# Kernel tuning notes

Hardware: AMD Instinct MI355X
Metric: run time of the kernel (lower is better)

The kernel has to match this reference:

```python
import jax, jax.numpy as jnp
from jax import lax
import numpy as np

B, C, L, HOP = 16, 64, 16384, 256
KS = 3        # LVC / conv kernel size
DIL = 3       # static Conv1d dilation (init arg)
KL = L // HOP # kernel_length (number of conditioning frames)


def setup_inputs() -> dict:
    key = jax.random.key(0)
    k0, k1, k2, k3 = jax.random.split(key, 4)
    return {
        "hidden_states": jax.random.normal(k0, (B, C, L), jnp.float32),
        "kernel": jax.random.normal(k1, (B, C, 2 * C, KS, KL), jnp.float32) * 0.05,
        "bias": jax.random.normal(k2, (B, 2 * C, KL), jnp.float32) * 0.05,
        "conv_w": jax.random.normal(k3, (C, C, KS), jnp.float32) * 0.05,
        "conv_b": jnp.zeros((C,), jnp.float32),
        "hop_size": HOP,
    }


def _lvc(x, kernel, bias, hop_size):
    # location-variable convolution; forward() uses dilation=1 here
    b, c, length = x.shape
    _, _, out_ch, ksize, klen = kernel.shape
    pad = (ksize - 1) // 2
    xp = jnp.pad(x, ((0, 0), (0, 0), (pad, pad)))
    # sliding windows of size ksize, stride 1 -> (b, c, length, ksize)
    win = jnp.stack([xp[:, :, i:i + length] for i in range(ksize)], axis=-1)
    # split time into (kernel_length, hop_size) frames
    win = win.reshape(b, c, klen, hop_size, ksize)
    # per-frame conv kernel contraction
    o = jnp.einsum('bilsk,biokl->bols', win, kernel)  # (b, out_ch, klen, hop)
    o = o + bias[:, :, :, None]
    return o.reshape(b, out_ch, klen * hop_size)


def reference(hidden_states, kernel, bias, conv_w, conv_b, hop_size):
    slope = 0.2
    pad = DIL * (KS - 1) // 2
    residual = hidden_states
    h = jax.nn.leaky_relu(hidden_states, slope)
    h = lax.conv_general_dilated(
        h, conv_w, window_strides=(1,), padding=[(pad, pad)],
        rhs_dilation=(DIL,), dimension_numbers=('NCH', 'OIH', 'NCH'))
    h = h + conv_b[None, :, None]
    h = jax.nn.leaky_relu(h, slope)
    h = _lvc(h, kernel, bias, hop_size)
    c = residual.shape[1]
    h = jax.nn.sigmoid(h[:, :c, :]) * jnp.tanh(h[:, c:, :])  # GLU gate
    return residual + h
```

## Files before the change

### kernel.cpp

```cpp
#include <hip/hip_runtime.h>
#include <hip/hip_bf16.h>

#define TB 256

typedef __attribute__((ext_vector_type(8))) short short8;
typedef __attribute__((ext_vector_type(4))) unsigned int uint4v;
typedef __attribute__((ext_vector_type(4))) float f32x4;

#define KTF_BYTES 50331648ull
#define WS_NEED   (KTF_BYTES + 24576ull)

static __device__ __forceinline__ float lrelu(float v){ return v > 0.f ? v : 0.2f*v; }

static __device__ __forceinline__ unsigned int pack2(float lo, float hi){
    __hip_bfloat162 h = __float22bfloat162_rn(float2{lo, hi});
    unsigned int r;
    __builtin_memcpy(&r, &h, 4);
    return r;
}

static __device__ __forceinline__ float bf2f(unsigned int u16v){
    return __uint_as_float(u16v << 16);
}

static __device__ __forceinline__ float glu_gate(float a, float t){
    t = fminf(fmaxf(t, -10.f), 10.f);
    float u = __expf(-a);
    float v = __expf(2.0f * t);
    float den = (1.0f + u) * (v + 1.0f);
    return (v - 1.0f) * __builtin_amdgcn_rcpf(den);
}


__global__ __launch_bounds__(256, 4)
void ktf_transpose(const float* __restrict__ kern, unsigned int* __restrict__ ktf)
{
    __shared__ unsigned int tl32[128 * 65];
    const int tid = threadIdx.x;
    const int blk = blockIdx.x;
    const int k   = blk % 3;
    const int ci2 = (blk / 3) % 32;
    const int b   = blk / 96;
    const int kk  = k*2 + (ci2 >> 4);
    const int hi  = (ci2 >> 2) & 3;
    const int jp  = ci2 & 3;

    const float* src0 = kern + (size_t)b*1572864 + (size_t)ci2*49152 + k*64;
    #pragma unroll
    for (int it = 0; it < 8; ++it) {
        int p = tid + it*TB;
        int oc = p >> 4, fq = p & 15;
        const float* s = src0 + oc*192 + fq*4;
        float4 v0 = *(const float4*)(s);
        float4 v1 = *(const float4*)(s + 24576);
        unsigned int* d = tl32 + oc*65 + fq*4;
        d[0] = pack2(v0.x, v1.x);
        d[1] = pack2(v0.y, v1.y);
        d[2] = pack2(v0.z, v1.z);
        d[3] = pack2(v0.w, v1.w);
    }
    __syncthreads();

    const int l = tid & 63, wvv = tid >> 6;
    const int c = (kk*4 + jp)*4 + hi;
    const int oc0 = 2*l;
    const int slot0 = (oc0 < 64) ? ((oc0 >> 3)*16 + (oc0 & 7))
                                 : (((oc0 - 64) >> 3)*16 + 8 + ((oc0 - 64) & 7));
    unsigned int* dst = ktf + (size_t)(b*96 + c)*8192 + slot0;
    const int f0 = wvv*16;
    #pragma unroll
    for (int fi = 0; fi < 16; ++fi) {
        int f = f0 + fi;
        uint2 v;
        v.x = tl32[(oc0    )*65 + f];
        v.y = tl32[(oc0 + 1)*65 + f];
        *(uint2*)(dst + f*128) = v;
    }
}

__global__ __launch_bounds__(256, 4)
void wf_prep(const float* __restrict__ conv_w, unsigned int* __restrict__ wf)
{
    int u = blockIdx.x*TB + threadIdx.x;
    int ln = u & 63, mt = (u >> 6) & 3, jp = (u >> 8) & 3, kk = u >> 10;
    int lo = ln & 15, hi = ln >> 4;
    int m  = mt*16 + lo;
    int k  = kk >> 1, ci = (kk & 1)*32 + hi*8 + jp*2;
    float a0 = conv_w[m*192 + ci*3 + k];
    float a1 = conv_w[m*192 + (ci + 1)*3 + k];
    wf[u] = pack2(a0, a1);
}

#define LDS_HT   18432
#define LDS_BIAS 36864

__global__ __launch_bounds__(512, 6)
void fused_kernel(const float* __restrict__ x,
                  const float* __restrict__ bias,
                  const float* __restrict__ conv_b,
                  const unsigned int* __restrict__ ktf,
                  const unsigned int* __restrict__ wf,
                  float* __restrict__ out)
{
    __shared__ char lds[37376];
    float* bias_lds = (float*)(lds + LDS_BIAS);

    const int tid = threadIdx.x;
    const int blk = blockIdx.x;
    const int h = blk & 1;
    const int bf = blk >> 1;
    const int b = bf >> 6, f = bf & 63;
    const int t0 = f << 8;
    const int tb = t0 + h*128;
    const int ln = tid & 63, wv = tid >> 6;
    const int lo = ln & 15, hi = ln >> 4;
    const int mt = wv & 3, nth = wv >> 2;

    if (tid < 128) bias_lds[tid] = bias[(size_t)b*8192 + tid*64 + f];

    {
        const float* xb = x + ((size_t)b*64 + wv*8) * 16384;
        const int ts = tb - 12;
        const bool interior = (ts >= 0) & (ts + 143 < 16384);
        #pragma unroll
        for (int it = 0; it < 3; ++it) {
            int p = (it < 2) ? (ln + it*64) : (128 + ln);
            if (it < 2 || ln < 16) {
                int t = ts + p;
                float v[8];
                if (interior) {
                    #pragma unroll
                    for (int j = 0; j < 8; ++j) v[j] = xb[j*16384 + t];
                } else {
                    bool ok = (unsigned)t < 16384u;
                    #pragma unroll
                    for (int j = 0; j < 8; ++j) v[j] = ok ? xb[j*16384 + t] : 0.f;
                }
                unsigned int w0 = pack2(lrelu(v[0]), lrelu(v[1]));
                unsigned int w1 = pack2(lrelu(v[2]), lrelu(v[3]));
                unsigned int w2 = pack2(lrelu(v[4]), lrelu(v[5]));
                unsigned int w3 = pack2(lrelu(v[6]), lrelu(v[7]));
                int a = (p*128 + wv*16) ^ ((p & 7) << 4);
                *(uint4*)(lds + a) = make_uint4(w0, w1, w2, w3);
            }
        }
    }
    __syncthreads();

    {
        uint4v aw[6];
        #pragma unroll
        for (int kk = 0; kk < 6; ++kk) {
            int w0 = kk*1024 + mt*64 + ln;
            aw[kk].x = wf[w0      ]; aw[kk].y = wf[w0 + 256];
            aw[kk].z = wf[w0 + 512]; aw[kk].w = wf[w0 + 768];
        }
        float4 cb4 = *(const float4*)(conv_b + mt*16 + hi*4);
        const int n0  = nth ? 5 : 0;
        const int cnt = nth ? 4 : 5;
        int bqa[6];
        #pragma unroll
        for (int kk = 0; kk < 6; ++kk) {
            int row = n0*16 + lo + 3*(kk >> 1) + 1;
            int cib = (kk & 1)*32 + hi*8;
            bqa[kk] = (row*128 + cib*2) ^ ((row & 7) << 4);
        }
        int hta = LDS_HT + (((n0*16 + lo)*128 + (mt*16 + hi*4)*2) ^ ((lo & 7) << 4));
        int pos = tb + n0*16 + lo - 8;
        #pragma unroll 1
        for (int i = 0; i < cnt; ++i) {
            f32x4 acc = {0.f, 0.f, 0.f, 0.f};
            __builtin_amdgcn_s_setprio(1);
            #pragma unroll
            for (int kk = 0; kk < 6; ++kk) {
                short8 bq = *(const short8*)(lds + bqa[kk]);
                acc = __builtin_amdgcn_mfma_f32_16x16x32_bf16(
                        __builtin_bit_cast(short8, aw[kk]), bq, acc, 0, 0, 0);
            }
            __builtin_amdgcn_s_setprio(0);

            bool valid = (unsigned)pos < 16384u;
            unsigned int h01 = valid ? pack2(lrelu(acc[0] + cb4.x), lrelu(acc[1] + cb4.y)) : 0u;
            unsigned int h23 = valid ? pack2(lrelu(acc[2] + cb4.z), lrelu(acc[3] + cb4.w)) : 0u;
            unsigned int* d = (unsigned int*)(lds + hta);
            d[0] = h01; d[1] = h23;

            #pragma unroll
            for (int kk = 0; kk < 6; ++kk) bqa[kk] += 2048;
            hta += 2048; pos += 16;
        }
    }
    __syncthreads();

    {
        uint4v am[6];
        const unsigned int* kp = ktf + (size_t)b*786432 + hi*8192 + f*128 + wv*16 + lo;
        #pragma unroll
        for (int kk = 0; kk < 6; ++kk) {
            int o = kk*131072;
            am[kk].x = kp[o        ]; am[kk].y = kp[o + 32768];
            am[kk].z = kp[o + 65536]; am[kk].w = kp[o + 98304];
        }
        const int c0 = wv*8;
        const bool alane = hi < 2;
        const int chA = alane ? (c0 + hi*4) : (c0 + (hi - 2)*4 + 2);
        float bs0 = bias_lds[chA],      bs1 = bias_lds[chA + 1];
        float bt0 = bias_lds[chA + 64], bt1 = bias_lds[chA + 65];

        int bqa[6];
        #pragma unroll
        for (int kk = 0; kk < 6; ++kk) {
            int row = lo + 7 + (kk >> 1);
            int cib = (kk & 1)*32 + hi*8;
            bqa[kk] = LDS_HT + ((row*128 + cib*2) ^ ((row & 7) << 4));
        }
        int q  = lo + 12;
        int ra = (q*128 + chA*2) ^ ((q & 7) << 4);
        float* ob = out + ((size_t)b*64 + chA)*16384 + tb + lo;

        #pragma unroll 1
        for (int i = 0; i < 8; ++i) {
            f32x4 acc = {0.f, 0.f, 0.f, 0.f};
            __builtin_amdgcn_s_setprio(1);
            #pragma unroll
            for (int kk = 0; kk < 6; ++kk) {
                short8 bq = *(const short8*)(lds + bqa[kk]);
                acc = __builtin_amdgcn_mfma_f32_16x16x32_bf16(
                        __builtin_bit_cast(short8, am[kk]), bq, acc, 0, 0, 0);
            }
            __builtin_amdgcn_s_setprio(0);

            float q1 = alane ? acc[2] : acc[0];
            float q2 = alane ? acc[3] : acc[1];
            float r1 = __shfl_xor(q1, 32, 64);
            float r2 = __shfl_xor(q2, 32, 64);
            float sig0 = alane ? acc[0] : r1;
            float tan0 = alane ? r1 : acc[2];
            float sig1 = alane ? acc[1] : r2;
            float tan1 = alane ? r2 : acc[3];

            unsigned int rv = *(const unsigned int*)(lds + ra);
            float h0 = bf2f(rv & 0xFFFFu), h1 = bf2f(rv >> 16);
            float xr0 = h0 > 0.f ? h0 : 5.0f*h0;
            float xr1 = h1 > 0.f ? h1 : 5.0f*h1;

            float g0 = glu_gate(sig0 + bs0, tan0 + bt0);
            float g1 = glu_gate(sig1 + bs1, tan1 + bt1);
            ob[(size_t)i*16]           = xr0 + g0;
            ob[16384 + (size_t)i*16]   = xr1 + g1;

            #pragma unroll
            for (int kk = 0; kk < 6; ++kk) bqa[kk] += 2048;
            ra += 2048;
        }
    }
}

extern "C" void kernel_launch(void* const* d_in, const int* in_sizes, int n_in,
                              void* d_out, int out_size, void* d_ws, size_t ws_size,
                              hipStream_t stream)
{
    const float* x      = (const float*)d_in[0];
    const float* kern   = (const float*)d_in[1];
    const float* bias   = (const float*)d_in[2];
    const float* conv_b = (const float*)d_in[4];
    float* out = (float*)d_out;

    if (ws_size < WS_NEED) return;

    unsigned int* ktf = (unsigned int*)d_ws;
    unsigned int* wf  = (unsigned int*)((char*)d_ws + KTF_BYTES);

    wf_prep      <<<dim3(24),   dim3(TB), 0, stream>>>((const float*)d_in[3], wf);
    ktf_transpose<<<dim3(1536), dim3(TB), 0, stream>>>(kern, ktf);
    fused_kernel <<<dim3(2048), dim3(512), 0, stream>>>(x, bias, conv_b, ktf, wf, out);
    (void)in_sizes; (void)n_in; (void)out_size;
}
```

Before: 85.36 us.

## Switch conv and LVC matmuls to 32x32x16 MFMA with new operand layouts

Both the dilated conv stage and the per-frame LVC contraction now use 32x32x16 bf16 MFMA tiles instead of 16x16x32. The weight-prep and kernel-transpose kernels are rewritten so each lane fetches its A operand as one 16-byte vector load. The sigmoid and tanh rows now land in the same lane, which removes the cross-lane shuffle in the GLU epilogue. The intent is fewer MFMA issues, fewer scattered global loads and a cheaper epilogue. In exchange the accumulators grow to 16 registers, launch bounds occupancy drops from 6 to 4, the LDS swizzle changes, and the conv stage now computes padded extra rows.

```diff
diff --git a/kernel.cpp b/kernel.cpp
--- a/kernel.cpp
+++ b/kernel.cpp
@@ -1,11 +1,9 @@
 #include <hip/hip_runtime.h>
 #include <hip/hip_bf16.h>
 
-#define TB 256
-
-typedef __attribute__((ext_vector_type(8))) short short8;
-typedef __attribute__((ext_vector_type(4))) unsigned int uint4v;
-typedef __attribute__((ext_vector_type(4))) float f32x4;
+typedef __attribute__((ext_vector_type(8)))  short        short8;
+typedef __attribute__((ext_vector_type(4)))  unsigned int uint4v;
+typedef __attribute__((ext_vector_type(16))) float        f32x16;
 
 #define KTF_BYTES 50331648ull
 #define WS_NEED   (KTF_BYTES + 24576ull)
@@ -33,99 +31,100 @@
 
 
 __global__ __launch_bounds__(256, 4)
-void ktf_transpose(const float* __restrict__ kern, unsigned int* __restrict__ ktf)
-{
-    __shared__ unsigned int tl32[128 * 65];
+void ktf_transpose(const float* __restrict__ kern, uint4v* __restrict__ ktf)
+{
+    __shared__ unsigned int tl[8704];
     const int tid = threadIdx.x;
     const int blk = blockIdx.x;
-    const int k   = blk % 3;
-    const int ci2 = (blk / 3) % 32;
+    const int r96 = blk % 96;
     const int b   = blk / 96;
-    const int kk  = k*2 + (ci2 >> 4);
-    const int hi  = (ci2 >> 2) & 3;
-    const int jp  = ci2 & 3;
-
-    const float* src0 = kern + (size_t)b*1572864 + (size_t)ci2*49152 + k*64;
+    const int k   = r96 >> 5;
+    const int ci8 = (r96 >> 2) & 7;
+    const int fq  = r96 & 3;
+
+    const float* src0 = kern + (size_t)b*1572864 + k*64 + fq*16;
     #pragma unroll
     for (int it = 0; it < 8; ++it) {
-        int p = tid + it*TB;
-        int oc = p >> 4, fq = p & 15;
-        const float* s = src0 + oc*192 + fq*4;
+        int u = tid + it*256;
+        int clp = u >> 9, oc = (u >> 2) & 127, f4 = u & 3;
+        int ci0 = ci8*8 + clp*2;
+        const float* s = src0 + (size_t)ci0*24576 + oc*192 + f4*4;
         float4 v0 = *(const float4*)(s);
         float4 v1 = *(const float4*)(s + 24576);
-        unsigned int* d = tl32 + oc*65 + fq*4;
-        d[0] = pack2(v0.x, v1.x);
-        d[1] = pack2(v0.y, v1.y);
-        d[2] = pack2(v0.z, v1.z);
-        d[3] = pack2(v0.w, v1.w);
+        unsigned int* d = tl + (oc*17 + f4*4)*4 + clp;
+        d[0]  = pack2(v0.x, v1.x);
+        d[4]  = pack2(v0.y, v1.y);
+        d[8]  = pack2(v0.z, v1.z);
+        d[12] = pack2(v0.w, v1.w);
     }
     __syncthreads();
 
-    const int l = tid & 63, wvv = tid >> 6;
-    const int c = (kk*4 + jp)*4 + hi;
-    const int oc0 = 2*l;
-    const int slot0 = (oc0 < 64) ? ((oc0 >> 3)*16 + (oc0 & 7))
-                                 : (((oc0 - 64) >> 3)*16 + 8 + ((oc0 - 64) & 7));
-    unsigned int* dst = ktf + (size_t)(b*96 + c)*8192 + slot0;
-    const int f0 = wvv*16;
+    const int ks  = k*4 + (ci8 >> 1);
+    const int hi1 = ci8 & 1;
     #pragma unroll
-    for (int fi = 0; fi < 16; ++fi) {
-        int f = f0 + fi;
-        uint2 v;
-        v.x = tl32[(oc0    )*65 + f];
-        v.y = tl32[(oc0 + 1)*65 + f];
-        *(uint2*)(dst + f*128) = v;
+    for (int it = 0; it < 2; ++it) {
+        int u = tid + it*256;
+        int col = u & 31, fi = u >> 5;
+        int f = fq*16 + fi;
+        #pragma unroll
+        for (int mt = 0; mt < 4; ++mt) {
+            int oc = (col < 16) ? (mt*16 + col) : (64 + mt*16 + (col - 16));
+            uint4v v = *(const uint4v*)(tl + (oc*17 + fi)*4);
+            size_t dst = ((size_t)((b*48 + mt*12 + ks)*64 + f))*64 + hi1*32 + col;
+            ktf[dst] = v;
+        }
     }
 }
 
 __global__ __launch_bounds__(256, 4)
-void wf_prep(const float* __restrict__ conv_w, unsigned int* __restrict__ wf)
-{
-    int u = blockIdx.x*TB + threadIdx.x;
-    int ln = u & 63, mt = (u >> 6) & 3, jp = (u >> 8) & 3, kk = u >> 10;
-    int lo = ln & 15, hi = ln >> 4;
-    int m  = mt*16 + lo;
-    int k  = kk >> 1, ci = (kk & 1)*32 + hi*8 + jp*2;
-    float a0 = conv_w[m*192 + ci*3 + k];
-    float a1 = conv_w[m*192 + (ci + 1)*3 + k];
-    wf[u] = pack2(a0, a1);
-}
-
-#define LDS_HT   18432
-#define LDS_BIAS 36864
-
-__global__ __launch_bounds__(512, 6)
+void wf_prep(const float* __restrict__ conv_w, uint4v* __restrict__ wf)
+{
+    int u = blockIdx.x*256 + threadIdx.x;
+    if (u >= 1536) return;
+    int l = u & 63, ks = (u >> 6) % 12, m = u / 768;
+    int col = l & 31, hi1 = l >> 5;
+    int oc = m*32 + col, k = ks >> 2, cib = (ks & 3)*16 + hi1*8;
+    uint4v v;
+    #pragma unroll
+    for (int jp = 0; jp < 4; ++jp) {
+        int ci = cib + 2*jp;
+        v[jp] = pack2(conv_w[oc*192 + ci*3 + k], conv_w[oc*192 + ci*3 + 3 + k]);
+    }
+    wf[u] = v;
+}
+
+#define HT_OFF   19456
+#define BIAS_OFF 39936
+
+__global__ __launch_bounds__(512, 4)
 void fused_kernel(const float* __restrict__ x,
                   const float* __restrict__ bias,
                   const float* __restrict__ conv_b,
-                  const unsigned int* __restrict__ ktf,
-                  const unsigned int* __restrict__ wf,
+                  const uint4v* __restrict__ ktf,
+                  const uint4v* __restrict__ wf,
                   float* __restrict__ out)
 {
-    __shared__ char lds[37376];
-    float* bias_lds = (float*)(lds + LDS_BIAS);
+    __shared__ char lds[40448];
+    float* bias_lds = (float*)(lds + BIAS_OFF);
 
     const int tid = threadIdx.x;
     const int blk = blockIdx.x;
-    const int h = blk & 1;
-    const int bf = blk >> 1;
+    const int h = blk & 1, bf = blk >> 1;
     const int b = bf >> 6, f = bf & 63;
-    const int t0 = f << 8;
-    const int tb = t0 + h*128;
+    const int tb = (f << 8) + h*128;
     const int ln = tid & 63, wv = tid >> 6;
-    const int lo = ln & 15, hi = ln >> 4;
-    const int mt = wv & 3, nth = wv >> 2;
+    const int col = ln & 31, hi1 = ln >> 5;
 
     if (tid < 128) bias_lds[tid] = bias[(size_t)b*8192 + tid*64 + f];
 
     {
         const float* xb = x + ((size_t)b*64 + wv*8) * 16384;
         const int ts = tb - 12;
-        const bool interior = (ts >= 0) & (ts + 143 < 16384);
+        const bool interior = (ts >= 0) & (ts + 151 < 16384);
         #pragma unroll
         for (int it = 0; it < 3; ++it) {
-            int p = (it < 2) ? (ln + it*64) : (128 + ln);
-            if (it < 2 || ln < 16) {
+            int p = ln + it*64;
+            if (it < 2 || ln < 24) {
                 int t = ts + p;
                 float v[8];
                 if (interior) {
@@ -136,122 +135,113 @@
                     #pragma unroll
                     for (int j = 0; j < 8; ++j) v[j] = ok ? xb[j*16384 + t] : 0.f;
                 }
-                unsigned int w0 = pack2(lrelu(v[0]), lrelu(v[1]));
-                unsigned int w1 = pack2(lrelu(v[2]), lrelu(v[3]));
-                unsigned int w2 = pack2(lrelu(v[4]), lrelu(v[5]));
-                unsigned int w3 = pack2(lrelu(v[6]), lrelu(v[7]));
-                int a = (p*128 + wv*16) ^ ((p & 7) << 4);
-                *(uint4*)(lds + a) = make_uint4(w0, w1, w2, w3);
+                uint4v w;
+                w[0] = pack2(lrelu(v[0]), lrelu(v[1]));
+                w[1] = pack2(lrelu(v[2]), lrelu(v[3]));
+                w[2] = pack2(lrelu(v[4]), lrelu(v[5]));
+                w[3] = pack2(lrelu(v[6]), lrelu(v[7]));
+                int a = p*128 + ((wv ^ (p & 7)) << 4);
+                *(uint4v*)(lds + a) = w;
             }
         }
     }
     __syncthreads();
 
     {
-        uint4v aw[6];
-        #pragma unroll
-        for (int kk = 0; kk < 6; ++kk) {
-            int w0 = kk*1024 + mt*64 + ln;
-            aw[kk].x = wf[w0      ]; aw[kk].y = wf[w0 + 256];
-            aw[kk].z = wf[w0 + 512]; aw[kk].w = wf[w0 + 768];
-        }
-        float4 cb4 = *(const float4*)(conv_b + mt*16 + hi*4);
-        const int n0  = nth ? 5 : 0;
-        const int cnt = nth ? 4 : 5;
-        int bqa[6];
-        #pragma unroll
-        for (int kk = 0; kk < 6; ++kk) {
-            int row = n0*16 + lo + 3*(kk >> 1) + 1;
-            int cib = (kk & 1)*32 + hi*8;
-            bqa[kk] = (row*128 + cib*2) ^ ((row & 7) << 4);
-        }
-        int hta = LDS_HT + (((n0*16 + lo)*128 + (mt*16 + hi*4)*2) ^ ((lo & 7) << 4));
-        int pos = tb + n0*16 + lo - 8;
+        const int m = wv & 1;
+        uint4v aw[12];
+        #pragma unroll
+        for (int ks = 0; ks < 12; ++ks)
+            aw[ks] = wf[(m*12 + ks)*64 + ln];
+        float4 cb[4];
+        #pragma unroll
+        for (int gq = 0; gq < 4; ++gq)
+            cb[gq] = *(const float4*)(conv_b + m*32 + (gq & 1)*8 + (gq >> 1)*16 + hi1*4);
+
         #pragma unroll 1
-        for (int i = 0; i < cnt; ++i) {
-            f32x4 acc = {0.f, 0.f, 0.f, 0.f};
+        for (int ti = wv; ti < 10; ti += 8) {
+            const int nt = ti >> 1;
+            const int prow = nt*32 + col;
+            f32x16 acc = {0,0,0,0,0,0,0,0,0,0,0,0,0,0,0,0};
             __builtin_amdgcn_s_setprio(1);
             #pragma unroll
-            for (int kk = 0; kk < 6; ++kk) {
-                short8 bq = *(const short8*)(lds + bqa[kk]);
-                acc = __builtin_amdgcn_mfma_f32_16x16x32_bf16(
-                        __builtin_bit_cast(short8, aw[kk]), bq, acc, 0, 0, 0);
+            for (int ks = 0; ks < 12; ++ks) {
+                int row  = prow + 3*(ks >> 2) + 1;
+                int slot = (ks & 3)*2 + hi1;
+                short8 bq = *(const short8*)(lds + row*128 + ((slot ^ (row & 7)) << 4));
+                acc = __builtin_amdgcn_mfma_f32_32x32x16_bf16(
+                        __builtin_bit_cast(short8, aw[ks]), bq, acc, 0, 0, 0);
             }
             __builtin_amdgcn_s_setprio(0);
 
-            bool valid = (unsigned)pos < 16384u;
-            unsigned int h01 = valid ? pack2(lrelu(acc[0] + cb4.x), lrelu(acc[1] + cb4.y)) : 0u;
-            unsigned int h23 = valid ? pack2(lrelu(acc[2] + cb4.z), lrelu(acc[3] + cb4.w)) : 0u;
-            unsigned int* d = (unsigned int*)(lds + hta);
-            d[0] = h01; d[1] = h23;
-
-            #pragma unroll
-            for (int kk = 0; kk < 6; ++kk) bqa[kk] += 2048;
-            hta += 2048; pos += 16;
+            if (prow < 144) {
+                int pos = tb + prow - 8;
+                bool valid = (unsigned)pos < 16384u;
+                #pragma unroll
+                for (int gq = 0; gq < 4; ++gq) {
+                    float v0 = lrelu(acc[gq*4 + 0] + cb[gq].x);
+                    float v1 = lrelu(acc[gq*4 + 1] + cb[gq].y);
+                    float v2 = lrelu(acc[gq*4 + 2] + cb[gq].z);
+                    float v3 = lrelu(acc[gq*4 + 3] + cb[gq].w);
+                    uint2 w;
+                    w.x = valid ? pack2(v0, v1) : 0u;
+                    w.y = valid ? pack2(v2, v3) : 0u;
+                    int slot16 = m*4 + (gq & 1) + (gq >> 1)*2;
+                    int addr = HT_OFF + prow*128 + ((slot16 ^ (prow & 7)) << 4) + hi1*8;
+                    *(uint2*)(lds + addr) = w;
+                }
+            }
         }
     }
     __syncthreads();
 
     {
-        uint4v am[6];
-        const unsigned int* kp = ktf + (size_t)b*786432 + hi*8192 + f*128 + wv*16 + lo;
-        #pragma unroll
-        for (int kk = 0; kk < 6; ++kk) {
-            int o = kk*131072;
-            am[kk].x = kp[o        ]; am[kk].y = kp[o + 32768];
-            am[kk].z = kp[o + 65536]; am[kk].w = kp[o + 98304];
-        }
-        const int c0 = wv*8;
-        const bool alane = hi < 2;
-        const int chA = alane ? (c0 + hi*4) : (c0 + (hi - 2)*4 + 2);
-        float bs0 = bias_lds[chA],      bs1 = bias_lds[chA + 1];
-        float bt0 = bias_lds[chA + 64], bt1 = bias_lds[chA + 65];
-
-        int bqa[6];
-        #pragma unroll
-        for (int kk = 0; kk < 6; ++kk) {
-            int row = lo + 7 + (kk >> 1);
-            int cib = (kk & 1)*32 + hi*8;
-            bqa[kk] = LDS_HT + ((row*128 + cib*2) ^ ((row & 7) << 4));
-        }
-        int q  = lo + 12;
-        int ra = (q*128 + chA*2) ^ ((q & 7) << 4);
-        float* ob = out + ((size_t)b*64 + chA)*16384 + tb + lo;
-
-        #pragma unroll 1
-        for (int i = 0; i < 8; ++i) {
-            f32x4 acc = {0.f, 0.f, 0.f, 0.f};
+        const int mt32 = wv & 3, nh = wv >> 2;
+        uint4v am[12];
+        const uint4v* kp = ktf + ((size_t)((b*48 + mt32*12)*64 + f))*64 + ln;
+        #pragma unroll
+        for (int ks = 0; ks < 12; ++ks)
+            am[ks] = kp[(size_t)ks*4096];
+        const int cA = mt32*16 + hi1*4;
+        float4 bs0 = *(const float4*)(bias_lds + cA);
+        float4 bs1 = *(const float4*)(bias_lds + cA + 8);
+        float4 bt0 = *(const float4*)(bias_lds + cA + 64);
+        float4 bt1 = *(const float4*)(bias_lds + cA + 72);
+        float* obase = out + ((size_t)b*64 + cA)*16384 + tb + col;
+        const int mslot = mt32*2;
+
+        #pragma unroll
+        for (int nt2 = 0; nt2 < 2; ++nt2) {
+            const int nt = nh*2 + nt2;
+            const int s = nt*32 + col;
+            f32x16 acc = {0,0,0,0,0,0,0,0,0,0,0,0,0,0,0,0};
             __builtin_amdgcn_s_setprio(1);
             #pragma unroll
-            for (int kk = 0; kk < 6; ++kk) {
-                short8 bq = *(const short8*)(lds + bqa[kk]);
-                acc = __builtin_amdgcn_mfma_f32_16x16x32_bf16(
-                        __builtin_bit_cast(short8, am[kk]), bq, acc, 0, 0, 0);
+            for (int ks = 0; ks < 12; ++ks) {
+                int row  = s + (ks >> 2) + 7;
+                int slot = (ks & 3)*2 + hi1;
+                short8 bq = *(const short8*)(lds + HT_OFF + row*128 + ((slot ^ (row & 7)) << 4));
+                acc = __builtin_amdgcn_mfma_f32_32x32x16_bf16(
+                        __builtin_bit_cast(short8, am[ks]), bq, acc, 0, 0, 0);
             }
             __builtin_amdgcn_s_setprio(0);
 
-            float q1 = alane ? acc[2] : acc[0];
-            float q2 = alane ? acc[3] : acc[1];
-            float r1 = __shfl_xor(q1, 32, 64);
-            float r2 = __shfl_xor(q2, 32, 64);
-            float sig0 = alane ? acc[0] : r1;
-            float tan0 = alane ? r1 : acc[2];
-            float sig1 = alane ? acc[1] : r2;
-            float tan1 = alane ? r2 : acc[3];
-
-            unsigned int rv = *(const unsigned int*)(lds + ra);
-            float h0 = bf2f(rv & 0xFFFFu), h1 = bf2f(rv >> 16);
-            float xr0 = h0 > 0.f ? h0 : 5.0f*h0;
-            float xr1 = h1 > 0.f ? h1 : 5.0f*h1;
-
-            float g0 = glu_gate(sig0 + bs0, tan0 + bt0);
-            float g1 = glu_gate(sig1 + bs1, tan1 + bt1);
-            ob[(size_t)i*16]           = xr0 + g0;
-            ob[16384 + (size_t)i*16]   = xr1 + g1;
+            int trow = s + 12;
+            uint2 rv0 = *(const uint2*)(lds + trow*128 + (( mslot      ^ (trow & 7)) << 4) + hi1*8);
+            uint2 rv1 = *(const uint2*)(lds + trow*128 + (((mslot + 1) ^ (trow & 7)) << 4) + hi1*8);
 
             #pragma unroll
-            for (int kk = 0; kk < 6; ++kk) bqa[kk] += 2048;
-            ra += 2048;
+            for (int r = 0; r < 8; ++r) {
+                float a = acc[r]     + ((r < 4) ? ((const float*)&bs0)[r] : ((const float*)&bs1)[r-4]);
+                float t = acc[r + 8] + ((r < 4) ? ((const float*)&bt0)[r] : ((const float*)&bt1)[r-4]);
+                unsigned int w = (r < 4) ? ((r < 2) ? rv0.x : rv0.y)
+                                         : ((r < 6) ? rv1.x : rv1.y);
+                unsigned int u16 = (r & 1) ? (w >> 16) : (w & 0xFFFFu);
+                float hv = bf2f(u16);
+                float xr = fminf(hv, 5.0f*hv);
+                float g  = glu_gate(a, t);
+                obase[(size_t)((r & 3) + 8*(r >> 2))*16384 + nt*32] = xr + g;
+            }
         }
     }
 }
@@ -268,11 +258,11 @@
 
     if (ws_size < WS_NEED) return;
 
-    unsigned int* ktf = (unsigned int*)d_ws;
-    unsigned int* wf  = (unsigned int*)((char*)d_ws + KTF_BYTES);
-
-    wf_prep      <<<dim3(24),   dim3(TB), 0, stream>>>((const float*)d_in[3], wf);
-    ktf_transpose<<<dim3(1536), dim3(TB), 0, stream>>>(kern, ktf);
+    uint4v* ktf = (uint4v*)d_ws;
+    uint4v* wf  = (uint4v*)((char*)d_ws + KTF_BYTES);
+
+    wf_prep      <<<dim3(6),    dim3(256), 0, stream>>>((const float*)d_in[3], wf);
+    ktf_transpose<<<dim3(1536), dim3(256), 0, stream>>>(kern, ktf);
     fused_kernel <<<dim3(2048), dim3(512), 0, stream>>>(x, bias, conv_b, ktf, wf, out);
     (void)in_sizes; (void)n_in; (void)out_size;
 }
```

New measurement: 99.66 us. +16.8%, slower.
